# Performance work log

Hardware: AMD Instinct MI355X
Metric: run time of the kernel (lower is better)

The kernel has to match this reference:

```python
import jax, jax.numpy as jnp
import numpy as np

OS_FACTOR = 1.5

def setup_inputs() -> dict:
    key = jax.random.key(0)
    k = jax.random.split(key, 5)
    B, T, I, H = 64, 1024, 1024, 1024
    s = 1.0 / np.sqrt(H).astype(np.float32)
    return {
        "x": jax.random.normal(k[0], (B, T, I), dtype=jnp.float32),
        "W_ih": jax.random.normal(k[1], (H, I), dtype=jnp.float32) * s,
        "W_hh": jax.random.normal(k[2], (H, H), dtype=jnp.float32) * s,
        "b_ih": jax.random.normal(k[3], (H,), dtype=jnp.float32) * s,
        "b_hh": jax.random.normal(k[4], (H,), dtype=jnp.float32) * s,
    }

def reference(x, W_ih, W_hh, b_ih, b_hh):
    B, T, I = x.shape
    H = W_hh.shape[0]
    delay_near = int(np.floor(OS_FACTOR))   # 1
    delay_far = int(np.ceil(OS_FACTOR))     # 2
    alpha = jnp.float32(OS_FACTOR - delay_near)  # 0.5
    # Precompute input projection for all steps (same math, batched GEMM): [T,B,H]
    xw = jnp.einsum('bti,hi->tbh', x, W_ih) + b_ih + b_hh
    # Circular delay buffer of the last `delay_far` states, zero-initialized.
    # In the torch code, negative indices into the zero `states` buffer read zeros,
    # which matches a zero-initialized buffer here.
    buf0 = jnp.zeros((delay_far, B, H), dtype=x.dtype)

    def step(buf, xw_t):
        # buf[-1] = state at t-1, buf[0] = state at t-delay_far
        h_read = (1.0 - alpha) * buf[delay_far - delay_near] + alpha * buf[0]
        h = jnp.tanh(xw_t + h_read @ W_hh.T)
        buf = jnp.concatenate([buf[1:], h[None]], axis=0)
        return buf, h

    _, states = jax.lax.scan(step, buf0, xw)   # states: [T,B,H]
    states = jnp.swapaxes(states, 0, 1)        # [B,T,H]
    h_final = states[:, -1, :][None]           # [1,B,H]
    return states, h_final
```

## Files before the change

### kernel.cpp

```cpp
#include <hip/hip_runtime.h>
#include <stdint.h>
#include <stddef.h>

#define TT 1024
#define BB 64
#define HH 1024
#define II 1024

typedef __attribute__((ext_vector_type(8))) short s16x8;
typedef __attribute__((ext_vector_type(4))) float f32x4;
typedef __attribute__((ext_vector_type(2))) unsigned u32x2;

#define WS_FLAGS 512
#define WS_RING  4096

static __device__ __forceinline__ unsigned short f2bf(float f) {
    union { float f; unsigned int u; } v; v.f = f;
    return (unsigned short)((v.u + 0x7fffu + ((v.u >> 16) & 1u)) >> 16);
}

static __device__ __forceinline__ s16x8 pack8(float4 a, float4 b) {
    s16x8 v;
    v[0] = (short)f2bf(a.x); v[1] = (short)f2bf(a.y);
    v[2] = (short)f2bf(a.z); v[3] = (short)f2bf(a.w);
    v[4] = (short)f2bf(b.x); v[5] = (short)f2bf(b.y);
    v[6] = (short)f2bf(b.z); v[7] = (short)f2bf(b.w);
    return v;
}

static __device__ __forceinline__ f32x4 zero4() {
    f32x4 v = {0.f, 0.f, 0.f, 0.f};
    return v;
}

static __device__ __forceinline__ s16x8 ld16_sc01(const void* p) {
    s16x8 v;
    asm volatile("global_load_dwordx4 %0, %1, off sc0 sc1" : "=v"(v) : "v"(p));
    return v;
}
static __device__ __forceinline__ unsigned ld4_sc01_wait(const void* p) {
    unsigned v;
    asm volatile("global_load_dword %0, %1, off sc0 sc1\n\ts_waitcnt vmcnt(0)"
                 : "=v"(v) : "v"(p) : "memory");
    return v;
}
static __device__ __forceinline__ void st8_sc01(void* p, u32x2 v) {
    asm volatile("global_store_dwordx2 %0, %1, off sc0 sc1" :: "v"(p), "v"(v) : "memory");
}
#define WAITV(n) do { asm volatile("s_waitcnt vmcnt(" #n ")" ::: "memory"); \
                      __builtin_amdgcn_sched_barrier(0); } while (0)

__global__ void init_ws(unsigned int* w) {
    for (int i = threadIdx.x; i < 640; i += 256)
        __hip_atomic_store(&w[i], 0u, __ATOMIC_RELAXED, __HIP_MEMORY_SCOPE_AGENT);
}

__global__ __launch_bounds__(256, 2) void xw_gemm(
    const float* __restrict__ X,
    const float* __restrict__ Wih,
    const float* __restrict__ bih,
    const float* __restrict__ bhh,
    float* __restrict__ out)
{
    __shared__ unsigned short As[128 * 64];
    __shared__ unsigned short Bs[128 * 64];

    const int tid  = threadIdx.x;
    const int lane = tid & 63;
    const int wid  = tid >> 6;
    const int bm = blockIdx.x >> 3;
    const int bn = blockIdx.x & 7;
    const size_t m0 = (size_t)bm * 128;
    const int n0 = bn * 128;
    const int wm = (wid >> 1) * 64;
    const int wn = (wid & 1) * 64;

    f32x4 acc[4][4];
#pragma unroll
    for (int i = 0; i < 4; ++i)
#pragma unroll
        for (int jj = 0; jj < 4; ++jj) acc[i][jj] = zero4();

    const int srow  = tid >> 1;
    const int shalf = tid & 1;
    const float* xp = X   + (m0 + srow) * (size_t)II + shalf * 32;
    const float* wp = Wih + (size_t)(n0 + srow) * II + shalf * 32;

    for (int kt = 0; kt < II / 64; ++kt) {
#pragma unroll
        for (int i = 0; i < 4; ++i) {
            float4 a0 = *(const float4*)(xp + i * 8);
            float4 a1 = *(const float4*)(xp + i * 8 + 4);
            float4 b0 = *(const float4*)(wp + i * 8);
            float4 b1 = *(const float4*)(wp + i * 8 + 4);
            const int c = shalf * 4 + i;
            const int cw = (c ^ (srow & 7)) << 3;
            *(s16x8*)&As[srow * 64 + cw] = pack8(a0, a1);
            *(s16x8*)&Bs[srow * 64 + cw] = pack8(b0, b1);
        }
        __syncthreads();

#pragma unroll
        for (int kk = 0; kk < 2; ++kk) {
            s16x8 af[4], bf[4];
            const int cs = kk * 4 + (lane >> 4);
#pragma unroll
            for (int mi = 0; mi < 4; ++mi) {
                const int r = wm + mi * 16 + (lane & 15);
                af[mi] = *(const s16x8*)&As[r * 64 + ((cs ^ (r & 7)) << 3)];
            }
#pragma unroll
            for (int ni = 0; ni < 4; ++ni) {
                const int r = wn + ni * 16 + (lane & 15);
                bf[ni] = *(const s16x8*)&Bs[r * 64 + ((cs ^ (r & 7)) << 3)];
            }
#pragma unroll
            for (int mi = 0; mi < 4; ++mi)
#pragma unroll
                for (int ni = 0; ni < 4; ++ni)
                    acc[mi][ni] = __builtin_amdgcn_mfma_f32_16x16x32_bf16(
                        af[mi], bf[ni], acc[mi][ni], 0, 0, 0);
        }
        __syncthreads();
        xp += 64; wp += 64;
    }

#pragma unroll
    for (int ni = 0; ni < 4; ++ni) {
        const int col = n0 + wn + ni * 16 + (lane & 15);
        const float bias = bih[col] + bhh[col];
#pragma unroll
        for (int mi = 0; mi < 4; ++mi) {
            const size_t row = m0 + wm + mi * 16 + ((lane >> 4) << 2);
#pragma unroll
            for (int r = 0; r < 4; ++r)
                out[(row + r) * (size_t)HH + col] = acc[mi][ni][r] + bias;
        }
    }
}

__global__ __launch_bounds__(256, 1) void rnn_scan(
    const float* __restrict__ Whh,
    float* __restrict__ out,
    void* __restrict__ ws)
{
    __shared__ unsigned short Hl[16 * 1024];

    const int tid  = threadIdx.x;
    const int lane = tid & 63;
    const int wid  = tid >> 6;
    const int g  = blockIdx.x >> 4;
    const int sl = blockIdx.x & 15;

    const int jb = sl * 64 + wid * 16;
    const int kg = lane >> 4;

    s16x8 afr[32];
    {
        const float* wr = Whh + (size_t)(jb + (lane & 15)) * HH + kg * 8;
#pragma unroll
        for (int c = 0; c < 32; ++c) {
            float4 p0 = *(const float4*)(wr + c * 32);
            float4 p1 = *(const float4*)(wr + c * 32 + 4);
            afr[c] = pack8(p0, p1);
        }
    }

    unsigned* fl = (unsigned*)((char*)ws + WS_FLAGS) + g * 64;
    char* rg = (char*)ws + WS_RING + (size_t)g * 65536;

    const int srow = tid >> 4;
    const int sseg = tid & 15;
    const char* sbase0 = rg + srow * 2048 + sseg * 16;
    const char* sbase1 = sbase0 + 32768;

    const int bl = lane & 15;
    const int b  = g * 16 + bl;
    const int f0 = jb + kg * 4;
    const int hrow = bl;

    float hprev[4];

    {
        const size_t idx = ((size_t)b * TT) * HH + f0;
        float4 xw4 = *(const float4*)(out + idx);
        float4 st;
        st.x = tanhf(xw4.x); st.y = tanhf(xw4.y);
        st.z = tanhf(xw4.z); st.w = tanhf(xw4.w);
        hprev[0] = st.x; hprev[1] = st.y; hprev[2] = st.z; hprev[3] = st.w;
        *(float4*)(out + idx) = st;
        u32x2 pk;
        pk[0] = (unsigned)f2bf(0.5f * st.x) | ((unsigned)f2bf(0.5f * st.y) << 16);
        pk[1] = (unsigned)f2bf(0.5f * st.z) | ((unsigned)f2bf(0.5f * st.w) << 16);
        st8_sc01(rg + 32768 + bl * 2048 + f0 * 2, pk);
    }
    asm volatile("s_waitcnt vmcnt(0)" ::: "memory");
    __syncthreads();
    if (tid == 0)
        __hip_atomic_store(&fl[sl], 1u, __ATOMIC_RELAXED, __HIP_MEMORY_SCOPE_AGENT);

#pragma unroll 1
    for (int t = 1; t < TT; ++t) {
        const size_t xidx = ((size_t)b * TT + t) * HH + f0;
        float4 xw4 = *(const float4*)(out + xidx);

        {
            const unsigned* myp = fl + (lane & 15);
            for (;;) {
                unsigned v = ld4_sc01_wait(myp);
                if (__all((int)(v >= (unsigned)t))) break;
                __builtin_amdgcn_s_sleep(1);
            }
            asm volatile("" ::: "memory");
            __builtin_amdgcn_sched_barrier(0);
        }

        {
            const char* sp = (t & 1) ? sbase1 : sbase0;
            s16x8 v[8];
#pragma unroll
            for (int i = 0; i < 8; ++i) v[i] = ld16_sc01(sp + i * 256);
#pragma unroll
            for (int i = 0; i < 8; ++i) {
                if (i == 0)      { WAITV(7); }
                else if (i == 1) { WAITV(6); }
                else if (i == 2) { WAITV(5); }
                else if (i == 3) { WAITV(4); }
                else if (i == 4) { WAITV(3); }
                else if (i == 5) { WAITV(2); }
                else if (i == 6) { WAITV(1); }
                else             { WAITV(0); }
                const int c = sseg + i * 16;
                *(s16x8*)&Hl[srow * 1024 + ((c ^ (srow & 7)) << 3)] = v[i];
            }
        }
        __syncthreads();

        f32x4 acc[4];
#pragma unroll
        for (int i = 0; i < 4; ++i) acc[i] = zero4();
#pragma unroll
        for (int kb = 0; kb < 4; ++kb) {
            s16x8 h8[8];
#pragma unroll
            for (int ki = 0; ki < 8; ++ki) {
                const int cs = (kb * 8 + ki) * 4 + kg;
                h8[ki] = *(const s16x8*)&Hl[hrow * 1024 + ((cs ^ (hrow & 7)) << 3)];
            }
#pragma unroll
            for (int ki = 0; ki < 8; ++ki)
                acc[ki & 3] = __builtin_amdgcn_mfma_f32_16x16x32_bf16(
                    afr[kb * 8 + ki], h8[ki], acc[ki & 3], 0, 0, 0);
        }
        f32x4 accT = acc[0] + acc[1] + acc[2] + acc[3];

        {
            float hn[4];
#pragma unroll
            for (int r = 0; r < 4; ++r)
                hn[r] = tanhf(accT[r] + ((const float*)&xw4)[r]);
            float4 st; st.x = hn[0]; st.y = hn[1]; st.z = hn[2]; st.w = hn[3];
            *(float4*)(out + xidx) = st;
            if (t == TT - 1) {
                *(float4*)(out + (size_t)BB * TT * HH + (size_t)b * HH + f0) = st;
            } else {
                u32x2 pk;
                pk[0] = (unsigned)f2bf(0.5f * (hn[0] + hprev[0])) |
                        ((unsigned)f2bf(0.5f * (hn[1] + hprev[1])) << 16);
                pk[1] = (unsigned)f2bf(0.5f * (hn[2] + hprev[2])) |
                        ((unsigned)f2bf(0.5f * (hn[3] + hprev[3])) << 16);
                char* rw = rg + (size_t)((t + 1) & 1) * 32768;
                st8_sc01(rw + bl * 2048 + f0 * 2, pk);
            }
#pragma unroll
            for (int r = 0; r < 4; ++r) hprev[r] = hn[r];
        }
        if (t < TT - 1) {
            asm volatile("s_waitcnt vmcnt(0)" ::: "memory");
            __syncthreads();
            if (tid == 0)
                __hip_atomic_store(&fl[sl], (unsigned)(t + 1),
                                   __ATOMIC_RELAXED, __HIP_MEMORY_SCOPE_AGENT);
        }
    }
}

extern "C" void kernel_launch(void* const* d_in, const int* in_sizes, int n_in,
                              void* d_out, int out_size, void* d_ws, size_t ws_size,
                              hipStream_t stream)
{
    const float* X   = (const float*)d_in[0];
    const float* Wih = (const float*)d_in[1];
    const float* Whh = (const float*)d_in[2];
    const float* bih = (const float*)d_in[3];
    const float* bhh = (const float*)d_in[4];
    float* out = (float*)d_out;

    init_ws<<<dim3(1), dim3(256), 0, stream>>>((unsigned int*)d_ws);
    xw_gemm<<<dim3(4096), dim3(256), 0, stream>>>(X, Wih, bih, bhh, out);
    rnn_scan<<<dim3(64), dim3(256), 0, stream>>>(Whh, out, d_ws);
}
```

Measured before the change: 3.855 ms.

## Split K across waves with LDS reduction, per-wave flags, fast tanh in RNN scan

The recurrent scan kernel now partitions the hidden-state reduction dimension across the four waves. Each wave loads only its K slice of the previous state directly from the global ring into registers, with no LDS staging copy, and overlaps the loads with MFMAs. Partial sums are reduced through a double-buffered LDS array. Per-wave completion flags replace the block-wide barrier plus a single flag, so fewer syncs sit on the serial critical path. tanhf is replaced with an exp2/rcp approximation, which trades some accuracy for fewer instructions.

New measurement: 5.441 ms. 1.41x slower.

```diff
diff --git a/kernel.cpp b/kernel.cpp
--- a/kernel.cpp
+++ b/kernel.cpp
@@ -33,6 +33,12 @@
     return v;
 }
 
+static __device__ __forceinline__ float tanh_fast(float x) {
+    float s = fminf(fmaxf(x, -9.0f), 9.0f);
+    float p = __builtin_amdgcn_exp2f(s * 2.885390081777927f);
+    return (p - 1.0f) * __builtin_amdgcn_rcpf(p + 1.0f);
+}
+
 static __device__ __forceinline__ s16x8 ld16_sc01(const void* p) {
     s16x8 v;
     asm volatile("global_load_dwordx4 %0, %1, off sc0 sc1" : "=v"(v) : "v"(p));
@@ -47,8 +53,6 @@
 static __device__ __forceinline__ void st8_sc01(void* p, u32x2 v) {
     asm volatile("global_store_dwordx2 %0, %1, off sc0 sc1" :: "v"(p), "v"(v) : "memory");
 }
-#define WAITV(n) do { asm volatile("s_waitcnt vmcnt(" #n ")" ::: "memory"); \
-                      __builtin_amdgcn_sched_barrier(0); } while (0)
 
 __global__ void init_ws(unsigned int* w) {
     for (int i = threadIdx.x; i < 640; i += 256)
@@ -139,12 +143,21 @@
     }
 }
 
+#define KSTEP(ki, n) do { \
+    asm volatile("s_waitcnt vmcnt(" #n ")" ::: "memory"); \
+    __builtin_amdgcn_sched_barrier(0); \
+    acc[0] = __builtin_amdgcn_mfma_f32_16x16x32_bf16(afr[0*8+(ki)], h8[ki], acc[0], 0, 0, 0); \
+    acc[1] = __builtin_amdgcn_mfma_f32_16x16x32_bf16(afr[1*8+(ki)], h8[ki], acc[1], 0, 0, 0); \
+    acc[2] = __builtin_amdgcn_mfma_f32_16x16x32_bf16(afr[2*8+(ki)], h8[ki], acc[2], 0, 0, 0); \
+    acc[3] = __builtin_amdgcn_mfma_f32_16x16x32_bf16(afr[3*8+(ki)], h8[ki], acc[3], 0, 0, 0); \
+} while (0)
+
 __global__ __launch_bounds__(256, 1) void rnn_scan(
     const float* __restrict__ Whh,
     float* __restrict__ out,
     void* __restrict__ ws)
 {
-    __shared__ unsigned short Hl[16 * 1024];
+    __shared__ float Red[2 * 16 * 64 * 4];
 
     const int tid  = threadIdx.x;
     const int lane = tid & 63;
@@ -152,32 +165,28 @@
     const int g  = blockIdx.x >> 4;
     const int sl = blockIdx.x & 15;
 
-    const int jb = sl * 64 + wid * 16;
     const int kg = lane >> 4;
+    const int bl = lane & 15;
 
     s16x8 afr[32];
-    {
-        const float* wr = Whh + (size_t)(jb + (lane & 15)) * HH + kg * 8;
-#pragma unroll
-        for (int c = 0; c < 32; ++c) {
-            float4 p0 = *(const float4*)(wr + c * 32);
-            float4 p1 = *(const float4*)(wr + c * 32 + 4);
-            afr[c] = pack8(p0, p1);
-        }
-    }
+#pragma unroll
+    for (int m = 0; m < 4; ++m)
+#pragma unroll
+        for (int ki = 0; ki < 8; ++ki) {
+            const float* wr = Whh + (size_t)(sl * 64 + m * 16 + bl) * HH
+                            + (wid * 8 + ki) * 32 + kg * 8;
+            afr[m * 8 + ki] = pack8(*(const float4*)wr, *(const float4*)(wr + 4));
+        }
 
     unsigned* fl = (unsigned*)((char*)ws + WS_FLAGS) + g * 64;
+    unsigned* myflag = fl + sl * 4 + wid;
     char* rg = (char*)ws + WS_RING + (size_t)g * 65536;
 
-    const int srow = tid >> 4;
-    const int sseg = tid & 15;
-    const char* sbase0 = rg + srow * 2048 + sseg * 16;
-    const char* sbase1 = sbase0 + 32768;
-
-    const int bl = lane & 15;
+    const char* const pb0 = rg + bl * 2048 + (wid * 32 + kg) * 16;
+    const char* const pb1 = pb0 + 32768;
+
     const int b  = g * 16 + bl;
-    const int f0 = jb + kg * 4;
-    const int hrow = bl;
+    const int f0 = sl * 64 + wid * 16 + kg * 4;
 
     float hprev[4];
 
@@ -185,8 +194,8 @@
         const size_t idx = ((size_t)b * TT) * HH + f0;
         float4 xw4 = *(const float4*)(out + idx);
         float4 st;
-        st.x = tanhf(xw4.x); st.y = tanhf(xw4.y);
-        st.z = tanhf(xw4.z); st.w = tanhf(xw4.w);
+        st.x = tanh_fast(xw4.x); st.y = tanh_fast(xw4.y);
+        st.z = tanh_fast(xw4.z); st.w = tanh_fast(xw4.w);
         hprev[0] = st.x; hprev[1] = st.y; hprev[2] = st.z; hprev[3] = st.w;
         *(float4*)(out + idx) = st;
         u32x2 pk;
@@ -195,9 +204,8 @@
         st8_sc01(rg + 32768 + bl * 2048 + f0 * 2, pk);
     }
     asm volatile("s_waitcnt vmcnt(0)" ::: "memory");
-    __syncthreads();
-    if (tid == 0)
-        __hip_atomic_store(&fl[sl], 1u, __ATOMIC_RELAXED, __HIP_MEMORY_SCOPE_AGENT);
+    if (lane == 0)
+        __hip_atomic_store(myflag, 1u, __ATOMIC_RELAXED, __HIP_MEMORY_SCOPE_AGENT);
 
 #pragma unroll 1
     for (int t = 1; t < TT; ++t) {
@@ -205,7 +213,7 @@
         float4 xw4 = *(const float4*)(out + xidx);
 
         {
-            const unsigned* myp = fl + (lane & 15);
+            const unsigned* myp = fl + lane;
             for (;;) {
                 unsigned v = ld4_sc01_wait(myp);
                 if (__all((int)(v >= (unsigned)t))) break;
@@ -215,50 +223,31 @@
             __builtin_amdgcn_sched_barrier(0);
         }
 
-        {
-            const char* sp = (t & 1) ? sbase1 : sbase0;
-            s16x8 v[8];
-#pragma unroll
-            for (int i = 0; i < 8; ++i) v[i] = ld16_sc01(sp + i * 256);
-#pragma unroll
-            for (int i = 0; i < 8; ++i) {
-                if (i == 0)      { WAITV(7); }
-                else if (i == 1) { WAITV(6); }
-                else if (i == 2) { WAITV(5); }
-                else if (i == 3) { WAITV(4); }
-                else if (i == 4) { WAITV(3); }
-                else if (i == 5) { WAITV(2); }
-                else if (i == 6) { WAITV(1); }
-                else             { WAITV(0); }
-                const int c = sseg + i * 16;
-                *(s16x8*)&Hl[srow * 1024 + ((c ^ (srow & 7)) << 3)] = v[i];
-            }
-        }
+        const char* p = (t & 1) ? pb1 : pb0;
+        s16x8 h8[8];
+#pragma unroll
+        for (int ki = 0; ki < 8; ++ki) h8[ki] = ld16_sc01(p + ki * 64);
+        f32x4 acc[4];
+#pragma unroll
+        for (int i = 0; i < 4; ++i) acc[i] = zero4();
+        KSTEP(0, 7); KSTEP(1, 6); KSTEP(2, 5); KSTEP(3, 4);
+        KSTEP(4, 3); KSTEP(5, 2); KSTEP(6, 1); KSTEP(7, 0);
+
+        float* rb = Red + (size_t)(t & 1) * 4096;
+#pragma unroll
+        for (int m = 0; m < 4; ++m)
+            *(f32x4*)&rb[((wid * 4 + m) * 64 + lane) * 4] = acc[m];
         __syncthreads();
-
-        f32x4 acc[4];
-#pragma unroll
-        for (int i = 0; i < 4; ++i) acc[i] = zero4();
-#pragma unroll
-        for (int kb = 0; kb < 4; ++kb) {
-            s16x8 h8[8];
-#pragma unroll
-            for (int ki = 0; ki < 8; ++ki) {
-                const int cs = (kb * 8 + ki) * 4 + kg;
-                h8[ki] = *(const s16x8*)&Hl[hrow * 1024 + ((cs ^ (hrow & 7)) << 3)];
-            }
-#pragma unroll
-            for (int ki = 0; ki < 8; ++ki)
-                acc[ki & 3] = __builtin_amdgcn_mfma_f32_16x16x32_bf16(
-                    afr[kb * 8 + ki], h8[ki], acc[ki & 3], 0, 0, 0);
-        }
-        f32x4 accT = acc[0] + acc[1] + acc[2] + acc[3];
+        f32x4 s4 = *(f32x4*)&rb[((0 * 4 + wid) * 64 + lane) * 4];
+#pragma unroll
+        for (int w2 = 1; w2 < 4; ++w2)
+            s4 = s4 + *(f32x4*)&rb[((w2 * 4 + wid) * 64 + lane) * 4];
 
         {
             float hn[4];
 #pragma unroll
             for (int r = 0; r < 4; ++r)
-                hn[r] = tanhf(accT[r] + ((const float*)&xw4)[r]);
+                hn[r] = tanh_fast(s4[r] + ((const float*)&xw4)[r]);
             float4 st; st.x = hn[0]; st.y = hn[1]; st.z = hn[2]; st.w = hn[3];
             *(float4*)(out + xidx) = st;
             if (t == TT - 1) {
@@ -277,9 +266,8 @@
         }
         if (t < TT - 1) {
             asm volatile("s_waitcnt vmcnt(0)" ::: "memory");
-            __syncthreads();
-            if (tid == 0)
-                __hip_atomic_store(&fl[sl], (unsigned)(t + 1),
+            if (lane == 0)
+                __hip_atomic_store(myflag, (unsigned)(t + 1),
                                    __ATOMIC_RELAXED, __HIP_MEMORY_SCOPE_AGENT);
         }
     }
```
